# Kernel optimization log

Measured on AMD Instinct MI355X. Metric: run time of the kernel, lower is better.

The kernel has to match this reference:

```python
import jax, jax.numpy as jnp
import numpy as np


def _rot_grids(group_order, ks, dtype):
    """Normalized sampling grids for each rotation (align_corners=False convention)."""
    k = jnp.arange(group_order, dtype=dtype)
    theta = 2.0 * jnp.pi * k / group_order                      # [G]
    c, s = jnp.cos(theta), jnp.sin(theta)
    # F.affine_grid base coords with align_corners=False: centers of pixels in [-1,1]
    lin = (jnp.arange(ks, dtype=dtype) + 0.5) * (2.0 / ks) - 1.0
    y, x = jnp.meshgrid(lin, lin, indexing='ij')                 # [ks,ks] each
    # theta rows: [cos, -sin, 0], [sin, cos, 0] applied to (x, y, 1)
    gx = c[:, None, None] * x - s[:, None, None] * y             # [G,ks,ks]
    gy = s[:, None, None] * x + c[:, None, None] * y             # [G,ks,ks]
    return gx, gy


def _grid_sample_bilinear_zeros(img, gx, gy):
    """Bilinear grid_sample, padding_mode='zeros', align_corners=False.
    img: [C,H,W]; gx,gy: [G,H,W] normalized coords. Returns [C,G,H,W]."""
    C, H, W = img.shape
    dt = img.dtype
    # unnormalize (align_corners=False)
    ix = ((gx + 1.0) * W - 1.0) * 0.5
    iy = ((gy + 1.0) * H - 1.0) * 0.5
    ix0 = jnp.floor(ix)
    iy0 = jnp.floor(iy)
    wx1 = (ix - ix0).astype(dt); wx0 = 1.0 - wx1
    wy1 = (iy - iy0).astype(dt); wy0 = 1.0 - wy1

    def gather(iyf, ixf):
        xi = ixf.astype(jnp.int32)
        yi = iyf.astype(jnp.int32)
        valid = ((xi >= 0) & (xi < W) & (yi >= 0) & (yi < H)).astype(dt)
        xi_c = jnp.clip(xi, 0, W - 1)
        yi_c = jnp.clip(yi, 0, H - 1)
        return img[:, yi_c, xi_c] * valid                        # [C,G,H,W]

    out = (gather(iy0, ix0) * (wy0 * wx0)
           + gather(iy0, ix0 + 1.0) * (wy0 * wx1)
           + gather(iy0 + 1.0, ix0) * (wy1 * wx0)
           + gather(iy0 + 1.0, ix0 + 1.0) * (wy1 * wx1))
    return out


def setup_inputs() -> dict:
    key = jax.random.key(0)
    out_ch, in_ch, ks = 512, 256, 9
    base_weight = jax.random.normal(key, (out_ch, in_ch, ks, ks), dtype=jnp.float32)
    return {"base_weight": base_weight, "group_order": 8}


def reference(base_weight, group_order):
    O, I, ks, _ = base_weight.shape
    img = base_weight.reshape(O * I, ks, ks)                     # [C,H,W]
    gx, gy = _rot_grids(group_order, ks, base_weight.dtype)      # [G,ks,ks]
    out = _grid_sample_bilinear_zeros(img, gx, gy)               # [C,G,ks,ks]
    # concat over rotations along dim 0 -> [G*O, I, ks, ks]
    out = out.reshape(O, I, group_order, ks, ks).transpose(2, 0, 1, 3, 4)
    return out.reshape(group_order * O, I, ks, ks)
```

## Files before the change

kernel.cpp:

```cpp
#include <hip/hip_runtime.h>


#define KS    9
#define NPIX  81
#define NC    64
#define BLOCK 256
#define NSLOT ((NC * NPIX) / 4)

typedef float f4 __attribute__((ext_vector_type(4)));

struct Tap { int qA, qB; float w0, w1, w2, w3; };

constexpr double SQ2H = 0.70710678118654752440084436210485;
constexpr double CS[8] = {1.0,  SQ2H, 0.0, -SQ2H, -1.0, -SQ2H,  0.0,  SQ2H};
constexpr double SN[8] = {0.0,  SQ2H, 1.0,  SQ2H,  0.0, -SQ2H, -1.0, -SQ2H};

constexpr int cfloor(double v) { int i = (int)v; return (v < (double)i) ? i - 1 : i; }

constexpr Tap mk(int g, int p) {
    int py = p / KS, px = p - KS * py;
    double lx = ((double)px + 0.5) * (2.0 / KS) - 1.0;
    double ly = ((double)py + 0.5) * (2.0 / KS) - 1.0;
    double gx = CS[g] * lx - SN[g] * ly;
    double gy = SN[g] * lx + CS[g] * ly;
    double ix = ((gx + 1.0) * KS - 1.0) * 0.5;
    double iy = ((gy + 1.0) * KS - 1.0) * 0.5;
    int x0 = cfloor(ix), y0 = cfloor(iy);
    double fx = ix - x0, fy = iy - y0;
    double wx0 = 1.0 - fx, wx1 = fx;
    double pw0 = 0.0, pw1 = 0.0; int xs = 0;
    if (x0 >= 0 && x0 < KS - 1)      { xs = x0;     pw0 = wx0; pw1 = wx1; }
    else if (x0 == KS - 1)           { xs = KS - 2; pw0 = 0.0; pw1 = wx0; }
    else if (x0 == -1)               { xs = 0;      pw0 = wx1; pw1 = 0.0; }
    int yA = y0, yB = y0 + 1;
    double wyA = (yA >= 0 && yA < KS) ? (1.0 - fy) : 0.0;
    double wyB = (yB >= 0 && yB < KS) ? fy : 0.0;
    int yAc = yA < 0 ? 0 : (yA > KS - 1 ? KS - 1 : yA);
    int yBc = yB < 0 ? 0 : (yB > KS - 1 ? KS - 1 : yB);
    return Tap{ yAc * KS + xs, yBc * KS + xs,
                (float)(wyA * pw0), (float)(wyA * pw1),
                (float)(wyB * pw0), (float)(wyB * pw1) };
}

struct TapTab { Tap t[8][NPIX]; };
constexpr TapTab build_tab() {
    TapTab T{};
    for (int g = 0; g < 8; ++g)
        for (int p = 0; p < NPIX; ++p) T.t[g][p] = mk(g, p);
    return T;
}
constexpr TapTab TT = build_tab();

__device__ __forceinline__ void bar_lds() {
    __builtin_amdgcn_sched_barrier(0);
    asm volatile("s_waitcnt lgkmcnt(0)" ::: "memory");
    __builtin_amdgcn_s_barrier();
    __builtin_amdgcn_sched_barrier(0);
}

template<int G, int P>
__device__ __forceinline__ void one_out(const float* lrow, float* otrow) {
    constexpr Tap t = TT.t[G][P];
    float v = 0.0f;
    if constexpr (t.w0 != 0.0f) v += lrow[t.qA]     * t.w0;
    if constexpr (t.w1 != 0.0f) v += lrow[t.qA + 1] * t.w1;
    if constexpr (t.w2 != 0.0f) v += lrow[t.qB]     * t.w2;
    if constexpr (t.w3 != 0.0f) v += lrow[t.qB + 1] * t.w3;
    otrow[P] = v;
}

template<int G, int P0, int NP>
__device__ __forceinline__ void compute_range(const float* lrow, float* otrow) {
    if constexpr (NP > 0) {
        one_out<G, P0>(lrow, otrow);
        compute_range<G, P0 + 1, NP - 1>(lrow, otrow);
    }
}

template<int G>
__device__ __forceinline__ void compute_quarter(int gq, const float* lrow,
                                                float* otrow) {
    if (gq == 0)      compute_range<G,  0, 20>(lrow, otrow);
    else if (gq == 1) compute_range<G, 20, 20>(lrow, otrow);
    else if (gq == 2) compute_range<G, 40, 20>(lrow, otrow);
    else              compute_range<G, 60, 21>(lrow, otrow);
}

__device__ __forceinline__ void cp_of(int d, int& c, int& p) {
    c = (d * 6473) >> 19;
    p = d - NPIX * c;
}

template<int G>
__device__ __forceinline__ int qe(int p) {
    if constexpr (G == 0) return p;
    else if constexpr (G == 4) return 80 - p;
    else {
        int py = (p * 57) >> 9;
        int px = p - KS * py;
        if constexpr (G == 2) return KS * px + 8 - py;
        else                  return 72 - KS * px + py;
    }
}

template<int G>
__device__ __forceinline__ void do_even(const float* lin, f4* d4, int t) {
    if constexpr (G == 0) {
        const f4* s4 = (const f4*)lin;
        for (int j = t; j < NSLOT; j += BLOCK) d4[j] = s4[j];
    } else {
        for (int j = t; j < NSLOT; j += BLOCK) {
            int d0 = 4 * j;
            f4 v;
#pragma unroll
            for (int k = 0; k < 4; ++k) {
                int c, p; cp_of(d0 + k, c, p);
                v[k] = lin[c * NPIX + qe<G>(p)];
            }
            d4[j] = v;
        }
    }
}

__device__ __forceinline__ void flush_ot(const float* ot, f4* d4, int t) {
    const f4* s4 = (const f4*)ot;
    for (int j = t; j < NSLOT; j += BLOCK) d4[j] = s4[j];
}

__global__ __launch_bounds__(BLOCK) void st_rotate(
        const float* __restrict__ in, float* __restrict__ out, int C) {
    __shared__ __align__(16) float lin[NC * NPIX];
    __shared__ __align__(16) float ot[NC * NPIX];
    const int t = threadIdx.x;
    const int c0 = blockIdx.x * NC;

    {
        const f4* src = (const f4*)(in + (size_t)c0 * NPIX);
        f4* dst = (f4*)lin;
        for (int j = t; j < NSLOT; j += BLOCK) dst[j] = src[j];
    }
    bar_lds();

    f4* const ob = (f4*)(out + (size_t)c0 * NPIX);
    const size_t gs4 = (size_t)C * NPIX / 4;

    do_even<0>(lin, ob + 0 * gs4, t);
    do_even<2>(lin, ob + 2 * gs4, t);
    do_even<4>(lin, ob + 4 * gs4, t);
    do_even<6>(lin, ob + 6 * gs4, t);

    const int c = t & 63, gq = t >> 6;
    const float* lrow = &lin[c * NPIX];
    float* otrow = &ot[c * NPIX];

    compute_quarter<1>(gq, lrow, otrow);
    bar_lds();
    flush_ot(ot, ob + 1 * gs4, t);
    bar_lds();
    compute_quarter<3>(gq, lrow, otrow);
    bar_lds();
    flush_ot(ot, ob + 3 * gs4, t);
    bar_lds();
    compute_quarter<5>(gq, lrow, otrow);
    bar_lds();
    flush_ot(ot, ob + 5 * gs4, t);
    bar_lds();
    compute_quarter<7>(gq, lrow, otrow);
    bar_lds();
    flush_ot(ot, ob + 7 * gs4, t);
}

extern "C" void kernel_launch(void* const* d_in, const int* in_sizes, int n_in,
                              void* d_out, int out_size, void* d_ws, size_t ws_size,
                              hipStream_t stream) {
    const float* in = (const float*)d_in[0];
    float* out = (float*)d_out;
    const int C = in_sizes[0] / NPIX;
    st_rotate<<<C / NC, BLOCK, 0, stream>>>(in, out, C);
}
```

Measured before the change: 365.8 us.

## Shrink blocks to a single wave of 16 channels and drop workgroup barriers

```diff
diff --git a/kernel.cpp b/kernel.cpp
--- a/kernel.cpp
+++ b/kernel.cpp
@@ -3,9 +3,10 @@
 
 #define KS    9
 #define NPIX  81
-#define NC    64
-#define BLOCK 256
-#define NSLOT ((NC * NPIX) / 4)
+#define NCW   16
+#define BLOCK 64
+#define NDW   (NCW * NPIX)
+#define NS4   (NDW / 4)
 
 typedef float f4 __attribute__((ext_vector_type(4)));
 
@@ -51,10 +52,9 @@
 }
 constexpr TapTab TT = build_tab();
 
-__device__ __forceinline__ void bar_lds() {
+__device__ __forceinline__ void wave_fence() {
     __builtin_amdgcn_sched_barrier(0);
     asm volatile("s_waitcnt lgkmcnt(0)" ::: "memory");
-    __builtin_amdgcn_s_barrier();
     __builtin_amdgcn_sched_barrier(0);
 }
 
@@ -75,15 +75,6 @@
         one_out<G, P0>(lrow, otrow);
         compute_range<G, P0 + 1, NP - 1>(lrow, otrow);
     }
-}
-
-template<int G>
-__device__ __forceinline__ void compute_quarter(int gq, const float* lrow,
-                                                float* otrow) {
-    if (gq == 0)      compute_range<G,  0, 20>(lrow, otrow);
-    else if (gq == 1) compute_range<G, 20, 20>(lrow, otrow);
-    else if (gq == 2) compute_range<G, 40, 20>(lrow, otrow);
-    else              compute_range<G, 60, 21>(lrow, otrow);
 }
 
 __device__ __forceinline__ void cp_of(int d, int& c, int& p) {
@@ -107,9 +98,9 @@
 __device__ __forceinline__ void do_even(const float* lin, f4* d4, int t) {
     if constexpr (G == 0) {
         const f4* s4 = (const f4*)lin;
-        for (int j = t; j < NSLOT; j += BLOCK) d4[j] = s4[j];
+        for (int j = t; j < NS4; j += BLOCK) d4[j] = s4[j];
     } else {
-        for (int j = t; j < NSLOT; j += BLOCK) {
+        for (int j = t; j < NS4; j += BLOCK) {
             int d0 = 4 * j;
             f4 v;
 #pragma unroll
@@ -122,24 +113,36 @@
     }
 }
 
-__device__ __forceinline__ void flush_ot(const float* ot, f4* d4, int t) {
+template<int G>
+__device__ __forceinline__ void do_odd(const float* lin, float* ot,
+                                       f4* d4, int t) {
+    const int cl = t & 15;
+    const int pq = t >> 4;
+    const float* lrow = lin + cl * NPIX;
+    float* otrow = ot + cl * NPIX;
+    wave_fence();
+    if (pq == 0)      compute_range<G,  0, 20>(lrow, otrow);
+    else if (pq == 1) compute_range<G, 20, 20>(lrow, otrow);
+    else if (pq == 2) compute_range<G, 40, 20>(lrow, otrow);
+    else              compute_range<G, 60, 21>(lrow, otrow);
+    wave_fence();
     const f4* s4 = (const f4*)ot;
-    for (int j = t; j < NSLOT; j += BLOCK) d4[j] = s4[j];
+    for (int j = t; j < NS4; j += BLOCK) d4[j] = s4[j];
 }
 
 __global__ __launch_bounds__(BLOCK) void st_rotate(
         const float* __restrict__ in, float* __restrict__ out, int C) {
-    __shared__ __align__(16) float lin[NC * NPIX];
-    __shared__ __align__(16) float ot[NC * NPIX];
+    __shared__ __align__(16) float lin[NDW];
+    __shared__ __align__(16) float ot[NDW];
     const int t = threadIdx.x;
-    const int c0 = blockIdx.x * NC;
+    const int c0 = blockIdx.x * NCW;
 
     {
         const f4* src = (const f4*)(in + (size_t)c0 * NPIX);
         f4* dst = (f4*)lin;
-        for (int j = t; j < NSLOT; j += BLOCK) dst[j] = src[j];
+        for (int j = t; j < NS4; j += BLOCK) dst[j] = src[j];
     }
-    bar_lds();
+    wave_fence();
 
     f4* const ob = (f4*)(out + (size_t)c0 * NPIX);
     const size_t gs4 = (size_t)C * NPIX / 4;
@@ -149,25 +152,10 @@
     do_even<4>(lin, ob + 4 * gs4, t);
     do_even<6>(lin, ob + 6 * gs4, t);
 
-    const int c = t & 63, gq = t >> 6;
-    const float* lrow = &lin[c * NPIX];
-    float* otrow = &ot[c * NPIX];
-
-    compute_quarter<1>(gq, lrow, otrow);
-    bar_lds();
-    flush_ot(ot, ob + 1 * gs4, t);
-    bar_lds();
-    compute_quarter<3>(gq, lrow, otrow);
-    bar_lds();
-    flush_ot(ot, ob + 3 * gs4, t);
-    bar_lds();
-    compute_quarter<5>(gq, lrow, otrow);
-    bar_lds();
-    flush_ot(ot, ob + 5 * gs4, t);
-    bar_lds();
-    compute_quarter<7>(gq, lrow, otrow);
-    bar_lds();
-    flush_ot(ot, ob + 7 * gs4, t);
+    do_odd<1>(lin, ot, ob + 1 * gs4, t);
+    do_odd<3>(lin, ot, ob + 3 * gs4, t);
+    do_odd<5>(lin, ot, ob + 5 * gs4, t);
+    do_odd<7>(lin, ot, ob + 7 * gs4, t);
 }
 
 extern "C" void kernel_launch(void* const* d_in, const int* in_sizes, int n_in,
@@ -176,5 +164,5 @@
     const float* in = (const float*)d_in[0];
     float* out = (float*)d_out;
     const int C = in_sizes[0] / NPIX;
-    st_rotate<<<C / NC, BLOCK, 0, stream>>>(in, out, C);
+    st_rotate<<<C / NCW, BLOCK, 0, stream>>>(in, out, C);
 }
```

Measured after the change: 377.2 us. +3.1%, slower.
